# Kernel tuning notes

Hardware: AMD Instinct MI355X
Metric: run time of the kernel (lower is better)

The kernel has to match this reference:

```python
import jax, jax.numpy as jnp
import numpy as np

B, T, J, D_O = 32, 128, 16, 16
D, H, L, M = 256, 8, 4, 8
DH = D // H
GMAX = 5
MLP = 4 * D
NUM_JOINT = np.array([16, 12, 10, 14, 16, 8, 12, 16])
NUM_GLOBAL = np.array([4, 0, 3, 5, 2, 0, 4, 3])


def setup_inputs() -> dict:
    key = jax.random.key(0)
    it = iter(jax.random.split(key, 48))
    def nrm(shape, s):
        return jax.random.normal(next(it), shape, dtype=jnp.float32) * s
    obs = jax.random.normal(next(it), (B, T, J, D_O), dtype=jnp.float32)
    jtype = jax.random.randint(next(it), (B, T, J), 0, 3)
    slide_mask = jtype == 0
    hinge_mask = jtype == 1
    global_mask = jtype == 2
    act_mask = jax.random.randint(next(it), (B, T, J), 0, 2).astype(bool)
    morph_mask = jax.random.randint(next(it), (B, J, J), 0, 2).astype(bool) | jnp.eye(J, dtype=bool)[None]
    m_idx = jax.random.randint(next(it), (B,), 0, M)
    has_global = jnp.asarray(NUM_GLOBAL > 0)
    s = 0.02
    W_slide = nrm((2, D), s); b_slide = jnp.zeros((D,), jnp.float32)
    W_hinge = nrm((3, D), s); b_hinge = jnp.zeros((D,), jnp.float32)
    # per-morphology global projection, rows beyond num_global zeroed (padding)
    grow = jnp.arange(GMAX)[None, :] < jnp.asarray(NUM_GLOBAL)[:, None]
    W_global = nrm((M, GMAX, D), s) * grow[:, :, None]
    b_global = jnp.zeros((M, D), jnp.float32)
    W_act = nrm((1, D), s)  # actuator_embedding: Linear(1, D, bias=False)
    # per-morphology position embeddings, zero beyond num_joint (matches torch zeros init + slice assign)
    jrow = jnp.arange(J)[None, :] < jnp.asarray(NUM_JOINT)[:, None]
    pos_emb = nrm((M, J, D), 1.0) * jrow[:, :, None]
    ln1_w = jnp.ones((L, D), jnp.float32); ln1_b = jnp.zeros((L, D), jnp.float32)
    qkv_w = nrm((L, D, 3 * D), s); qkv_b = jnp.zeros((L, 3 * D), jnp.float32)
    proj_w = nrm((L, D, D), s); proj_b = jnp.zeros((L, D), jnp.float32)
    ln2_w = jnp.ones((L, D), jnp.float32); ln2_b = jnp.zeros((L, D), jnp.float32)
    fc1_w = nrm((L, D, MLP), s); fc1_b = jnp.zeros((L, MLP), jnp.float32)
    fc2_w = nrm((L, MLP, D), s); fc2_b = jnp.zeros((L, D), jnp.float32)
    ls1 = jnp.full((L, D), 1e-4, jnp.float32); ls2 = jnp.full((L, D), 1e-4, jnp.float32)
    return dict(obs=obs, slide_mask=slide_mask, hinge_mask=hinge_mask, global_mask=global_mask,
                act_mask=act_mask, morph_mask=morph_mask, m_idx=m_idx, has_global=has_global,
                W_slide=W_slide, b_slide=b_slide, W_hinge=W_hinge, b_hinge=b_hinge,
                W_global=W_global, b_global=b_global, W_act=W_act, pos_emb=pos_emb,
                ln1_w=ln1_w, ln1_b=ln1_b, qkv_w=qkv_w, qkv_b=qkv_b, proj_w=proj_w, proj_b=proj_b,
                ln2_w=ln2_w, ln2_b=ln2_b, fc1_w=fc1_w, fc1_b=fc1_b, fc2_w=fc2_w, fc2_b=fc2_b,
                ls1=ls1, ls2=ls2)


def _ln(x, w, b):
    m = x.mean(-1, keepdims=True)
    v = ((x - m) ** 2).mean(-1, keepdims=True)
    return (x - m) * jax.lax.rsqrt(v + 1e-5) * w + b


def reference(obs, slide_mask, hinge_mask, global_mask, act_mask, morph_mask, m_idx, has_global,
              W_slide, b_slide, W_hinge, b_hinge, W_global, b_global, W_act, pos_emb,
              ln1_w, ln1_b, qkv_w, qkv_b, proj_w, proj_b, ln2_w, ln2_b,
              fc1_w, fc1_b, fc2_w, fc2_b, ls1, ls2):
    # --- JointEmbedding (morphology-indexed expert selection, vectorized gather) ---
    emb_slide = obs[..., :2] @ W_slide + b_slide
    x = jnp.where(slide_mask[..., None], emb_slide, jnp.zeros_like(emb_slide))
    emb_hinge = obs[..., :3] @ W_hinge + b_hinge
    x = jnp.where(hinge_mask[..., None], emb_hinge, x)
    # per-sample expert weights gathered by m_idx; padded cols are zero so math matches per-expert in-dims
    emb_g = jnp.einsum('btjg,bgd->btjd', obs[..., :GMAX], W_global[m_idx]) + b_global[m_idx][:, None, None, :]
    gmask = global_mask & has_global[m_idx][:, None, None]  # experts with num_global==0 are skipped
    x = jnp.where(gmask[..., None], emb_g, x)
    # actuator embedding: Linear(1, D, bias=False) on 0/1 mask
    x = x + act_mask[..., None].astype(x.dtype) * W_act[0]
    # morphology-indexed position embedding (zero-padded beyond num_joint)
    x = x + pos_emb[m_idx][:, None]  # (B,1,J,D) broadcast over T
    # --- masked transformer over joints; (B T) flattening == broadcasting mask over T ---
    bias = jnp.where(morph_mask, 0.0, -1e9).astype(x.dtype)[:, None, None, :, :]  # (B,1,1,J,J)
    for l in range(L):
        h = _ln(x, ln1_w[l], ln1_b[l])
        qkv = h @ qkv_w[l] + qkv_b[l]
        q, k, v = jnp.split(qkv, 3, axis=-1)
        def heads(t):
            return t.reshape(B, T, J, H, DH).transpose(0, 1, 3, 2, 4)
        q, k, v = heads(q), heads(k), heads(v)
        scores = jnp.einsum('bthqd,bthkd->bthqk', q, k) * (DH ** -0.5) + bias
        a = jax.nn.softmax(scores, axis=-1)
        o = jnp.einsum('bthqk,bthkd->bthqd', a, v).transpose(0, 1, 3, 2, 4).reshape(B, T, J, D)
        x = x + ls1[l] * (o @ proj_w[l] + proj_b[l])
        h = _ln(x, ln2_w[l], ln2_b[l])
        x = x + ls2[l] * (jax.nn.gelu(h @ fc1_w[l] + fc1_b[l]) @ fc2_w[l] + fc2_b[l])
    return x
```

## Files before the change

### kernel.cpp

```cpp
#include <hip/hip_runtime.h>
#include <hip/hip_bf16.h>
#include <stdint.h>

typedef short bf16x8 __attribute__((ext_vector_type(8)));
typedef float f32x4 __attribute__((ext_vector_type(4)));

#define DI __device__ __forceinline__

DI unsigned short f2bf(float f) {
    return __builtin_bit_cast(unsigned short, __float2bfloat16(f));
}

DI unsigned char f2fp8(float f) {
    int p = __builtin_amdgcn_cvt_pk_fp8_f32(f, 0.f, 0, false);
    return (unsigned char)(p & 0xff);
}

DI f32x4 mfma16(bf16x8 a, bf16x8 b, f32x4 c) {
    return __builtin_amdgcn_mfma_f32_16x16x32_bf16(a, b, c, 0, 0, 0);
}

DI f32x4 mfma8(long a, long b, f32x4 c) {
    return __builtin_amdgcn_mfma_f32_16x16x32_fp8_fp8(a, b, c, 0, 0, 0);
}

DI void gload16c(const unsigned char* g, unsigned char* l) {
    __builtin_amdgcn_global_load_lds(
        (const __attribute__((address_space(1))) unsigned int*)g,
        (__attribute__((address_space(3))) unsigned int*)l, 16, 0, 0);
}

DI float gelu_s(float hv) {
    return hv / (1.0f + __expf(-1.702f * hv));
}

#define RSYNC0() do { asm volatile("s_waitcnt vmcnt(0)" ::: "memory"); \
    __builtin_amdgcn_s_barrier(); __builtin_amdgcn_sched_barrier(0); } while (0)

__global__ __launch_bounds__(256)
void prep_kernel(const float* __restrict__ qkv_w, const float* __restrict__ proj_w,
                 const float* __restrict__ fc1_w, const float* __restrict__ fc2_w,
                 const float* __restrict__ ls1, const float* __restrict__ ls2,
                 unsigned char* __restrict__ out)
{
    __shared__ float tileA[256][17];
    __shared__ float tileB[32][129];
    const int tid = threadIdx.x;
    const int tgl = blockIdx.x;
    const int layer = tgl / 192;
    const int tl = tgl % 192;
    bool kindA; const float* W; int ldN = 0, src_n16 = 0, strip = 0, ctb = 0;
    const float* lsp = nullptr;
    size_t off;
    if (tl < 64) {
        int h = tl >> 3, u = tl & 7;
        if (u < 6) { kindA = true;  W = qkv_w + (size_t)layer * 256 * 768; ldN = 768;
                     src_n16 = (u >> 1) * 16 + 2 * h + (u & 1);
                     off = (size_t)h * 40960 + (u < 4 ? u * 4096 : 16384 + (u - 4) * 4096); }
        else       { kindA = false; W = proj_w + (size_t)layer * 256 * 256; ldN = 256;
                     strip = 32 * h; ctb = (u - 6) * 8; lsp = ls1 + layer * 256;
                     off = (size_t)h * 40960 + 24576 + (size_t)(u - 6) * 8192; }
    } else {
        int q = tl - 64, rp = q >> 2, v = q & 3;
        if (v < 2) { kindA = true;  W = fc1_w + (size_t)layer * 256 * 1024; ldN = 1024;
                     src_n16 = 2 * rp + v;
                     off = 327680 + (size_t)rp * 24576 + (size_t)v * 4096; }
        else       { kindA = false; W = fc2_w + (size_t)layer * 1024 * 256; ldN = 256;
                     strip = 32 * rp; ctb = (v - 2) * 8; lsp = ls2 + layer * 256;
                     off = 327680 + (size_t)rp * 24576 + 8192 + (size_t)(v - 2) * 8192; }
    }
    off += (size_t)layer * 1114112;
    if (kindA) {
        const int cn = tid & 15, k0 = tid >> 4;
        const float* src = W + src_n16 * 16 + cn;
        #pragma unroll
        for (int p = 0; p < 16; ++p) {
            int kk = p * 16 + k0;
            tileA[kk][cn] = src[(size_t)kk * ldN];
        }
    } else {
        const int kk = tid >> 3, c0 = (tid & 7) * 16;
        const float* src = W + (size_t)(strip + kk) * ldN + ctb * 16 + c0;
        #pragma unroll
        for (int j = 0; j < 16; ++j) tileB[kk][c0 + j] = src[j];
    }
    __syncthreads();
    if (kindA) {
        unsigned char* dstb = out + off;
        int e0 = tid * 16;
        int s = e0 >> 9;
        int l = (e0 >> 3) & 63;
        union { unsigned char u[8]; unsigned long long v; } g0, g1;
        int kb0 = 32 * s + 8 * (l >> 4), n0 = l & 15;
        int kb1 = 32 * s + 8 * ((l + 1) >> 4), n1 = (l + 1) & 15;
        #pragma unroll
        for (int i = 0; i < 8; ++i) g0.u[i] = f2fp8(tileA[kb0 + i][n0]);
        #pragma unroll
        for (int i = 0; i < 8; ++i) g1.u[i] = f2fp8(tileA[kb1 + i][n1]);
        *(unsigned long long*)(dstb + e0) = g0.v;
        *(unsigned long long*)(dstb + e0 + 8) = g1.v;
    } else {
        unsigned short* dsts = (unsigned short*)(out + off);
        int e0 = tid * 16;
        int s = e0 >> 9;
        int l = (e0 >> 3) & 63;
        union { unsigned short u[8]; bf16x8 v; } pk;
        {
            int kb = 8 * (l >> 4);
            int cc = s * 16 + (l & 15);
            const float sc = lsp[ctb * 16 + cc];
            #pragma unroll
            for (int i = 0; i < 8; ++i) pk.u[i] = f2bf(tileB[kb + i][cc] * sc);
            *(bf16x8*)(dsts + e0) = pk.v;
        }
        int e1 = e0 + 8;
        int s1 = e1 >> 9;
        int l1 = (e1 >> 3) & 63;
        union { unsigned short u[8]; bf16x8 v; } pk1;
        {
            int kb = 8 * (l1 >> 4);
            int cc = s1 * 16 + (l1 & 15);
            const float sc = lsp[ctb * 16 + cc];
            #pragma unroll
            for (int i = 0; i < 8; ++i) pk1.u[i] = f2bf(tileB[kb + i][cc] * sc);
            *(bf16x8*)(dsts + e1) = pk1.v;
        }
    }
}

#define CAT_(a, b) a##b
#define CAT(a, b) CAT_(a, b)

#define F8N(F)      F(0)F(1)F(2)F(3)F(4)F(5)F(6)F(7)
#define F16N(F)     F(0)F(1)F(2)F(3)F(4)F(5)F(6)F(7)F(8)F(9)F(10)F(11)F(12)F(13)F(14)F(15)
#define F8A(F,a)    F(0,a)F(1,a)F(2,a)F(3,a)F(4,a)F(5,a)F(6,a)F(7,a)
#define F8H(F,a)    F(8,a)F(9,a)F(10,a)F(11,a)F(12,a)F(13,a)F(14,a)F(15,a)
#define F16A(F,a)   F8A(F,a) F8H(F,a)
#define F8B(F,a,b)  F(0,a,b)F(1,a,b)F(2,a,b)F(3,a,b)F(4,a,b)F(5,a,b)F(6,a,b)F(7,a,b)
#define F16C(F,a,b) F8B(F,a,b) F(8,a,b)F(9,a,b)F(10,a,b)F(11,a,b)F(12,a,b)F(13,a,b)F(14,a,b)F(15,a,b)

#define DECLX(n)  f32x4 CAT(xA,n);
#define DECLAV(s) long CAT(avA,s);

#define EMB_N(n, P, R) { const int col = (n)*16 + lq; float e = 0.f;            \
    if (sl_) e = o0_*W_slide[col] + o1_*W_slide[256+col] + b_slide[col];        \
    else if (hi_) e = o0_*W_hinge[col] + o1_*W_hinge[256+col]                   \
                    + o2_*W_hinge[512+col] + b_hinge[col];                      \
    else if (gl_) e = b_global[m*256+col]                                       \
        + o0_*W_global[(m*5+0)*256+col] + o1_*W_global[(m*5+1)*256+col]         \
        + o2_*W_global[(m*5+2)*256+col] + o3_*W_global[(m*5+3)*256+col]         \
        + o4_*W_global[(m*5+4)*256+col];                                        \
    if (am_) e += W_act[col];                                                   \
    e += pos_emb[pb_ + col];                                                    \
    CAT(CAT(x,P),n)[R] = e; }

#define EMB_ROW(R, G, P) { const int j_ = lg*4 + (R);                           \
    const size_t tok_ = (size_t)(G)*16 + j_;                                    \
    const float* ob_ = obs + tok_*16;                                           \
    const float o0_=ob_[0], o1_=ob_[1], o2_=ob_[2], o3_=ob_[3], o4_=ob_[4];     \
    const int sl_=slide_m[tok_], hi_=hinge_m[tok_];                             \
    const int gl_=global_m[tok_]&&hg; const int am_=act_m[tok_];                \
    const size_t pb_ = ((size_t)m*16+j_)*256;                                   \
    F16C(EMB_N, P, R) }

#define EMBED(G, P) { EMB_ROW(0,G,P) EMB_ROW(1,G,P) EMB_ROW(2,G,P) EMB_ROW(3,G,P) }

#define LNS_N(n, P) { f32x4 v4_ = CAT(CAT(x,P),n);                              \
    sm0+=v4_[0]; sq0+=v4_[0]*v4_[0]; sm1+=v4_[1]; sq1+=v4_[1]*v4_[1];           \
    sm2+=v4_[2]; sq2+=v4_[2]*v4_[2]; sm3+=v4_[3]; sq3+=v4_[3]*v4_[3]; }

#define RED4(v) { v+=__shfl_xor(v,1,64); v+=__shfl_xor(v,2,64);                 \
                  v+=__shfl_xor(v,4,64); v+=__shfl_xor(v,8,64); }

#define LNW_N(n, P) { const float wv_=lw_[(n)*16+lq], lbv_=lb_[(n)*16+lq];      \
    const int t16_=(2*(n)+(lq>>3))&3; const int base_=(((n)&7)>>1)*512+(lq&7);  \
    slotA8[base_+(4*lg+0+16*t16_)*8] = f2fp8((CAT(CAT(x,P),n)[0]-mu0)*rs0*wv_+lbv_); \
    slotA8[base_+(4*lg+1+16*t16_)*8] = f2fp8((CAT(CAT(x,P),n)[1]-mu1)*rs1*wv_+lbv_); \
    slotA8[base_+(4*lg+2+16*t16_)*8] = f2fp8((CAT(CAT(x,P),n)[2]-mu2)*rs2*wv_+lbv_); \
    slotA8[base_+(4*lg+3+16*t16_)*8] = f2fp8((CAT(CAT(x,P),n)[3]-mu3)*rs3*wv_+lbv_); }

#define LAYER_NORM(LW, LB, P) do {                                              \
    const float* lw_ = (LW); const float* lb_ = (LB);                           \
    float sm0=0,sm1=0,sm2=0,sm3=0, sq0=0,sq1=0,sq2=0,sq3=0;                     \
    F16A(LNS_N, P)                                                              \
    RED4(sm0) RED4(sm1) RED4(sm2) RED4(sm3)                                     \
    RED4(sq0) RED4(sq1) RED4(sq2) RED4(sq3)                                     \
    const float mu0=sm0*(1.f/256.f), mu1=sm1*(1.f/256.f);                       \
    const float mu2=sm2*(1.f/256.f), mu3=sm3*(1.f/256.f);                       \
    const float rs0=rsqrtf(sq0*(1.f/256.f)-mu0*mu0+1e-5f);                      \
    const float rs1=rsqrtf(sq1*(1.f/256.f)-mu1*mu1+1e-5f);                      \
    const float rs2=rsqrtf(sq2*(1.f/256.f)-mu2*mu2+1e-5f);                      \
    const float rs3=rsqrtf(sq3*(1.f/256.f)-mu3*mu3+1e-5f);                      \
    F8A(LNW_N, P)                                                               \
    CAT(CAT(av,P),0) = *(const long*)(slotA8 + 0*512 + lane*8);                 \
    CAT(CAT(av,P),1) = *(const long*)(slotA8 + 1*512 + lane*8);                 \
    CAT(CAT(av,P),2) = *(const long*)(slotA8 + 2*512 + lane*8);                 \
    CAT(CAT(av,P),3) = *(const long*)(slotA8 + 3*512 + lane*8);                 \
    F8H(LNW_N, P)                                                               \
    CAT(CAT(av,P),4) = *(const long*)(slotA8 + 0*512 + lane*8);                 \
    CAT(CAT(av,P),5) = *(const long*)(slotA8 + 1*512 + lane*8);                 \
    CAT(CAT(av,P),6) = *(const long*)(slotA8 + 2*512 + lane*8);                 \
    CAT(CAT(av,P),7) = *(const long*)(slotA8 + 3*512 + lane*8);                 \
} while (0)

#define MFKE(s, TB_) { ae = mfma8(CAT(avA,s), bfragW8((TB_),(s)), ae); }
#define MFKO(s, TB_) { aod = mfma8(CAT(avA,s), bfragW8((TB_),(s)), aod); }
#define MFK8F(TB_) MFKE(0,TB_) MFKO(1,TB_) MFKE(2,TB_) MFKO(3,TB_) \
                   MFKE(4,TB_) MFKO(5,TB_) MFKE(6,TB_) MFKO(7,TB_)

#define FOLD_CT(ct, SB, OF) {                                                   \
    bf16x8 bq_ = *(const bf16x8*)(dbuf + (SB) + ((ct)>>3)*8192                  \
                                  + ((ct)&7)*1024 + lane*16);                   \
    CAT(xA,ct) = mfma16((OF), bq_, CAT(xA,ct)); }

#define ADDB_N(n, OFS) { const float d_ = biasbuf[(OFS)+(n)*16+lq];             \
    CAT(xA,n)[0]+=d_; CAT(xA,n)[1]+=d_; CAT(xA,n)[2]+=d_; CAT(xA,n)[3]+=d_; }

#define STORE_N(n) {                                                            \
    op0[(lg*4+0)*256+(n)*16+lq]=CAT(xA,n)[0]; op0[(lg*4+1)*256+(n)*16+lq]=CAT(xA,n)[1]; \
    op0[(lg*4+2)*256+(n)*16+lq]=CAT(xA,n)[2]; op0[(lg*4+3)*256+(n)*16+lq]=CAT(xA,n)[3]; }

#define ATTN_ROUND(RR, BB) {                                                    \
    const int rg_ = layer * 24 + (RR);                                          \
    RSYNC0();                                                                   \
    if (rg_ + 1 < 96) stageRound(rg_ + 1);                                      \
    _Pragma("unroll")                                                           \
    for (int tt = 0; tt < 4; ++tt) {                                            \
        int sec = tt >> 1, nn = tt & 1;                                         \
        float bv = biasbuf[sec * 256 + (2 * (RR) + nn) * 16 + lq];              \
        f32x4 ae = {bv, bv, bv, bv}, aod = zf;                                  \
        MFK8F((BB) + tt * 4096)                                                 \
        f32x4 a0 = ae + aod;                                                    \
        unsigned short* dstl = sec ? ks : qp;                                   \
        _Pragma("unroll")                                                       \
        for (int rr = 0; rr < 4; ++rr)                                          \
            dstl[(4 * lg + rr) * 40 + nn * 16 + lq] = f2bf(a0[rr]);             \
    }                                                                           \
    _Pragma("unroll")                                                           \
    for (int tv = 0; tv < 2; ++tv) {                                            \
        float bv = biasbuf[512 + (2 * (RR) + tv) * 16 + lq];                    \
        f32x4 ae = {bv, bv, bv, bv}, aod = zf;                                  \
        MFK8F((BB) + 16384 + tv * 4096)                                         \
        f32x4 a0 = ae + aod;                                                    \
        _Pragma("unroll")                                                       \
        for (int rr = 0; rr < 4; ++rr)                                          \
            vT[(tv * 16 + lq) * 40 + 4 * lg + rr] = f2bf(a0[rr]);               \
    }                                                                           \
    { bf16x8 of_ = attn(); F16C(FOLD_CT, (BB) + 24576, of_) }                   \
}

#define MLP_ROUND(RR, BB) {                                                     \
    const int rg_ = layer * 24 + 8 + (RR);                                      \
    RSYNC0();                                                                   \
    if (rg_ + 1 < 96) stageRound(rg_ + 1);                                      \
    _Pragma("unroll")                                                           \
    for (int u = 0; u < 2; ++u) {                                               \
        const int ub_ = (BB) + u * 24576;                                       \
        const int rp_ = 2 * (RR) + u;                                           \
        _Pragma("unroll")                                                       \
        for (int tt = 0; tt < 2; ++tt) {                                        \
            float bv = biasbuf[768 + (2 * rp_ + tt) * 16 + lq];                 \
            f32x4 ae = {bv, bv, bv, bv}, aod = zf;                              \
            MFK8F(ub_ + tt * 4096)                                              \
            f32x4 a0 = ae + aod;                                                \
            int t16 = (2 * tt + (lq >> 3)) & 3;                                 \
            _Pragma("unroll")                                                   \
            for (int rr = 0; rr < 4; ++rr)                                      \
                ks[((4 * lg + rr) + 16 * t16) * 8 + (lq & 7)]                   \
                    = f2bf(gelu_s(a0[rr]));                                     \
        }                                                                       \
        bf16x8 gf_ = *(const bf16x8*)(ks + lane * 8);                           \
        F16C(FOLD_CT, ub_ + 8192, gf_)                                          \
    }                                                                           \
}

__global__ __launch_bounds__(512)
void fused_kernel(const float* __restrict__ obs, const int* __restrict__ slide_m,
                  const int* __restrict__ hinge_m, const int* __restrict__ global_m,
                  const int* __restrict__ act_m, const int* __restrict__ morph_m,
                  const int* __restrict__ m_idx, const int* __restrict__ has_g,
                  const float* __restrict__ W_slide, const float* __restrict__ b_slide,
                  const float* __restrict__ W_hinge, const float* __restrict__ b_hinge,
                  const float* __restrict__ W_global, const float* __restrict__ b_global,
                  const float* __restrict__ W_act, const float* __restrict__ pos_emb,
                  const float* __restrict__ ln1_w, const float* __restrict__ ln1_b,
                  const float* __restrict__ qkv_b, const float* __restrict__ proj_b,
                  const float* __restrict__ ln2_w, const float* __restrict__ ln2_b,
                  const float* __restrict__ fc1_b, const float* __restrict__ fc2_b,
                  const float* __restrict__ ls1, const float* __restrict__ ls2,
                  const unsigned char* __restrict__ wsb, float* __restrict__ out)
{
    __shared__ __align__(16) unsigned char smem[151552];
    unsigned char* dbuf = smem;
    float* bias_lds = (float*)(smem + 98304);
    float* biasbuf = (float*)(smem + 99328);
    const int tid = threadIdx.x;
    const int w = tid >> 6, lane = tid & 63, lq = lane & 15, lg = lane >> 4;
    unsigned char* pw = smem + 108544 + w * 5376;
    unsigned char* slotA8 = pw;
    unsigned short* qp = (unsigned short*)pw;
    unsigned short* ks = (unsigned short*)(pw + 1280);
    unsigned short* vT = (unsigned short*)(pw + 2560);

    const int G = blockIdx.x * 8 + w;
    const int b = blockIdx.x >> 4;
    const int m = m_idx[b];
    const int hg = has_g[m];

    auto bfragW8 = [&](int tb, int s) -> long {
        return *(const long*)(dbuf + tb + s * 512 + lane * 8);
    };
    auto stageRound = [&](int ri) {
        int lyr = ri / 24, rr = ri - lyr * 24;
        size_t off; int nld;
        if (rr < 8) { off = (size_t)lyr * 1114112 + (size_t)rr * 40960; nld = 5; }
        else        { off = (size_t)lyr * 1114112 + 327680 + (size_t)(rr - 8) * 49152;
                      nld = 6; }
        const unsigned char* src = wsb + off + tid * 16;
        unsigned char* dst = dbuf + (ri & 1) * 49152 + tid * 16;
        gload16c(src, dst);
        gload16c(src + 8192, dst + 8192);
        gload16c(src + 16384, dst + 16384);
        gload16c(src + 24576, dst + 24576);
        gload16c(src + 32768, dst + 32768);
        if (nld == 6) gload16c(src + 40960, dst + 40960);
    };

    stageRound(0);
    if (tid < 256) bias_lds[tid] = morph_m[b * 256 + tid] ? 0.0f : -1e9f;
    #pragma unroll
    for (int ii = 0; ii < 8; ++ii) {
        int idx = ii * 64 + lane;
        vT[(idx >> 4) * 40 + 16 + (idx & 15)] = 0;
    }

    F16N(DECLX)
    F8N(DECLAV)

    EMBED(G, A)

    const float SCALE = 0.17677669529663687f;
    const f32x4 zf = {0.f, 0.f, 0.f, 0.f};

    auto attn = [&]() -> bf16x8 {
        bf16x8 kf = *(const bf16x8*)(ks + lq * 40 + lg * 8);
        bf16x8 qf = *(const bf16x8*)(qp + lq * 40 + lg * 8);
        f32x4 st = mfma16(kf, qf, zf);
        float p0 = st[0] * SCALE + bias_lds[lq * 16 + 4 * lg + 0];
        float p1 = st[1] * SCALE + bias_lds[lq * 16 + 4 * lg + 1];
        float p2 = st[2] * SCALE + bias_lds[lq * 16 + 4 * lg + 2];
        float p3 = st[3] * SCALE + bias_lds[lq * 16 + 4 * lg + 3];
        float mx = fmaxf(fmaxf(p0, p1), fmaxf(p2, p3));
        mx = fmaxf(mx, __shfl_xor(mx, 16, 64));
        mx = fmaxf(mx, __shfl_xor(mx, 32, 64));
        p0 = __expf(p0 - mx); p1 = __expf(p1 - mx);
        p2 = __expf(p2 - mx); p3 = __expf(p3 - mx);
        float ps = p0 + p1 + p2 + p3;
        ps += __shfl_xor(ps, 16, 64);
        ps += __shfl_xor(ps, 32, 64);
        float inv = 1.f / ps;
        qp[lq * 40 + lg * 4 + 0] = f2bf(p0 * inv);
        qp[lq * 40 + lg * 4 + 1] = f2bf(p1 * inv);
        qp[lq * 40 + lg * 4 + 2] = f2bf(p2 * inv);
        qp[lq * 40 + lg * 4 + 3] = f2bf(p3 * inv);
        qp[lq * 40 + 16 + lg * 4 + 0] = 0;
        qp[lq * 40 + 16 + lg * 4 + 1] = 0;
        qp[lq * 40 + 16 + lg * 4 + 2] = 0;
        qp[lq * 40 + 16 + lg * 4 + 3] = 0;
        bf16x8 pf = *(const bf16x8*)(qp + lq * 40 + lg * 8);
        f32x4 o0 = mfma16(pf, *(const bf16x8*)(vT + lq * 40 + lg * 8), zf);
        f32x4 o1 = mfma16(pf, *(const bf16x8*)(vT + (16 + lq) * 40 + lg * 8), zf);
        #pragma unroll
        for (int rr = 0; rr < 4; ++rr) {
            ks[((4 * lg + rr) + 16 * ((lq >> 3) & 3)) * 8 + (lq & 7)] = f2bf(o0[rr]);
            ks[((4 * lg + rr) + 16 * ((2 + (lq >> 3)) & 3)) * 8 + (lq & 7)] = f2bf(o1[rr]);
        }
        return *(const bf16x8*)(ks + lane * 8);
    };

    for (int layer = 0; layer < 4; ++layer) {
        for (int i = tid; i < 2304; i += 512) {
            float v;
            if (i < 768)       v = qkv_b[layer * 768 + i];
            else if (i < 1792) v = fc1_b[layer * 1024 + i - 768];
            else if (i < 2048) v = ls1[layer * 256 + i - 1792] * proj_b[layer * 256 + i - 1792];
            else               v = ls2[layer * 256 + i - 2048] * fc2_b[layer * 256 + i - 2048];
            biasbuf[i] = v;
        }
        __syncthreads();

        LAYER_NORM(ln1_w + layer * 256, ln1_b + layer * 256, A);
        #pragma unroll
        for (int ii = 0; ii < 8; ++ii) {
            int idx = ii * 64 + lane;
            vT[(idx >> 4) * 40 + 16 + (idx & 15)] = 0;
        }
        F16A(ADDB_N, 1792)

        for (int hp = 0; hp < 4; ++hp) {
            ATTN_ROUND(2 * hp, 0)
            ATTN_ROUND(2 * hp + 1, 49152)
        }

        LAYER_NORM(ln2_w + layer * 256, ln2_b + layer * 256, A);
        F16A(ADDB_N, 2048)

        for (int mp = 0; mp < 8; ++mp) {
            MLP_ROUND(2 * mp, 0)
            MLP_ROUND(2 * mp + 1, 49152)
        }
    }

    float* op0 = out + (size_t)G * 4096;
    F16N(STORE_N)
}

extern "C" void kernel_launch(void* const* d_in, const int* in_sizes, int n_in,
                              void* d_out, int out_size, void* d_ws, size_t ws_size,
                              hipStream_t stream) {
    (void)in_sizes; (void)n_in; (void)out_size; (void)ws_size;
    const float* obs      = (const float*)d_in[0];
    const int*   slide_m  = (const int*)d_in[1];
    const int*   hinge_m  = (const int*)d_in[2];
    const int*   global_m = (const int*)d_in[3];
    const int*   act_m    = (const int*)d_in[4];
    const int*   morph_m  = (const int*)d_in[5];
    const int*   m_idx    = (const int*)d_in[6];
    const int*   has_g    = (const int*)d_in[7];
    const float* W_slide  = (const float*)d_in[8];
    const float* b_slide  = (const float*)d_in[9];
    const float* W_hinge  = (const float*)d_in[10];
    const float* b_hinge  = (const float*)d_in[11];
    const float* W_global = (const float*)d_in[12];
    const float* b_global = (const float*)d_in[13];
    const float* W_act    = (const float*)d_in[14];
    const float* pos_emb  = (const float*)d_in[15];
    const float* ln1_w    = (const float*)d_in[16];
    const float* ln1_b    = (const float*)d_in[17];
    const float* qkv_w    = (const float*)d_in[18];
    const float* qkv_b    = (const float*)d_in[19];
    const float* proj_w   = (const float*)d_in[20];
    const float* proj_b   = (const float*)d_in[21];
    const float* ln2_w    = (const float*)d_in[22];
    const float* ln2_b    = (const float*)d_in[23];
    const float* fc1_w    = (const float*)d_in[24];
    const float* fc1_b    = (const float*)d_in[25];
    const float* fc2_w    = (const float*)d_in[26];
    const float* fc2_b    = (const float*)d_in[27];
    const float* ls1      = (const float*)d_in[28];
    const float* ls2      = (const float*)d_in[29];
    unsigned char* wsb = (unsigned char*)d_ws;

    prep_kernel<<<768, 256, 0, stream>>>(qkv_w, proj_w, fc1_w, fc2_w, ls1, ls2, wsb);
    fused_kernel<<<512, 512, 0, stream>>>(obs, slide_m, hinge_m, global_m, act_m, morph_m,
        m_idx, has_g, W_slide, b_slide, W_hinge, b_hinge, W_global, b_global, W_act, pos_emb,
        ln1_w, ln1_b, qkv_b, proj_b, ln2_w, ln2_b, fc1_b, fc2_b, ls1, ls2, wsb, (float*)d_out);
}
```

Before: 618.4 us.

## Interleave FP8 weight fragments for 16-byte LDS loads and use four accumulators

The weight-prep kernel now writes the FP8 B-fragments so that k-slices 2p and 2p+1 for a lane sit next to each other. The main kernel can then fetch two fragments with one 16-byte LDS read instead of two 8-byte reads. The MFMA chain is also split across four accumulators instead of two, which shortens dependency chains. The cost is extra accumulator registers and a packed layout that the preprocessing and the consumer must agree on exactly.

Measured after the change: 621.6 us. About the same (+0.5%).

```diff
diff --git a/kernel.cpp b/kernel.cpp
--- a/kernel.cpp
+++ b/kernel.cpp
@@ -4,6 +4,7 @@
 
 typedef short bf16x8 __attribute__((ext_vector_type(8)));
 typedef float f32x4 __attribute__((ext_vector_type(4)));
+typedef long longx2 __attribute__((ext_vector_type(2)));
 
 #define DI __device__ __forceinline__
 
@@ -87,18 +88,17 @@
     __syncthreads();
     if (kindA) {
         unsigned char* dstb = out + off;
-        int e0 = tid * 16;
-        int s = e0 >> 9;
-        int l = (e0 >> 3) & 63;
+        const int p = tid >> 6, l = tid & 63;
+        const int s0 = 2 * p, s1 = 2 * p + 1;
         union { unsigned char u[8]; unsigned long long v; } g0, g1;
-        int kb0 = 32 * s + 8 * (l >> 4), n0 = l & 15;
-        int kb1 = 32 * s + 8 * ((l + 1) >> 4), n1 = (l + 1) & 15;
+        int kb0 = 32 * s0 + 8 * (l >> 4), n0 = l & 15;
+        int kb1 = 32 * s1 + 8 * (l >> 4), n1 = l & 15;
         #pragma unroll
         for (int i = 0; i < 8; ++i) g0.u[i] = f2fp8(tileA[kb0 + i][n0]);
         #pragma unroll
         for (int i = 0; i < 8; ++i) g1.u[i] = f2fp8(tileA[kb1 + i][n1]);
-        *(unsigned long long*)(dstb + e0) = g0.v;
-        *(unsigned long long*)(dstb + e0 + 8) = g1.v;
+        *(unsigned long long*)(dstb + tid * 16) = g0.v;
+        *(unsigned long long*)(dstb + tid * 16 + 8) = g1.v;
     } else {
         unsigned short* dsts = (unsigned short*)(out + off);
         int e0 = tid * 16;
@@ -203,10 +203,15 @@
     CAT(CAT(av,P),7) = *(const long*)(slotA8 + 3*512 + lane*8);                 \
 } while (0)
 
-#define MFKE(s, TB_) { ae = mfma8(CAT(avA,s), bfragW8((TB_),(s)), ae); }
-#define MFKO(s, TB_) { aod = mfma8(CAT(avA,s), bfragW8((TB_),(s)), aod); }
-#define MFK8F(TB_) MFKE(0,TB_) MFKO(1,TB_) MFKE(2,TB_) MFKO(3,TB_) \
-                   MFKE(4,TB_) MFKO(5,TB_) MFKE(6,TB_) MFKO(7,TB_)
+#define MFK8F(TB_) {                                                            \
+    longx2 b01_ = *(const longx2*)(dbuf + (TB_) + 0 * 1024 + lane * 16);        \
+    longx2 b23_ = *(const longx2*)(dbuf + (TB_) + 1 * 1024 + lane * 16);        \
+    longx2 b45_ = *(const longx2*)(dbuf + (TB_) + 2 * 1024 + lane * 16);        \
+    longx2 b67_ = *(const longx2*)(dbuf + (TB_) + 3 * 1024 + lane * 16);        \
+    ac0 = mfma8(avA0, b01_[0], ac0); ac1 = mfma8(avA1, b01_[1], ac1);           \
+    ac2 = mfma8(avA2, b23_[0], ac2); ac3 = mfma8(avA3, b23_[1], ac3);           \
+    ac0 = mfma8(avA4, b45_[0], ac0); ac1 = mfma8(avA5, b45_[1], ac1);           \
+    ac2 = mfma8(avA6, b67_[0], ac2); ac3 = mfma8(avA7, b67_[1], ac3); }
 
 #define FOLD_CT(ct, SB, OF) {                                                   \
     bf16x8 bq_ = *(const bf16x8*)(dbuf + (SB) + ((ct)>>3)*8192                  \
@@ -228,9 +233,9 @@
     for (int tt = 0; tt < 4; ++tt) {                                            \
         int sec = tt >> 1, nn = tt & 1;                                         \
         float bv = biasbuf[sec * 256 + (2 * (RR) + nn) * 16 + lq];              \
-        f32x4 ae = {bv, bv, bv, bv}, aod = zf;                                  \
+        f32x4 ac0 = {bv, bv, bv, bv}, ac1 = zf, ac2 = zf, ac3 = zf;             \
         MFK8F((BB) + tt * 4096)                                                 \
-        f32x4 a0 = ae + aod;                                                    \
+        f32x4 a0 = (ac0 + ac1) + (ac2 + ac3);                                   \
         unsigned short* dstl = sec ? ks : qp;                                   \
         _Pragma("unroll")                                                       \
         for (int rr = 0; rr < 4; ++rr)                                          \
@@ -239,9 +244,9 @@
     _Pragma("unroll")                                                           \
     for (int tv = 0; tv < 2; ++tv) {                                            \
         float bv = biasbuf[512 + (2 * (RR) + tv) * 16 + lq];                    \
-        f32x4 ae = {bv, bv, bv, bv}, aod = zf;                                  \
+        f32x4 ac0 = {bv, bv, bv, bv}, ac1 = zf, ac2 = zf, ac3 = zf;             \
         MFK8F((BB) + 16384 + tv * 4096)                                         \
-        f32x4 a0 = ae + aod;                                                    \
+        f32x4 a0 = (ac0 + ac1) + (ac2 + ac3);                                   \
         _Pragma("unroll")                                                       \
         for (int rr = 0; rr < 4; ++rr)                                          \
             vT[(tv * 16 + lq) * 40 + 4 * lg + rr] = f2bf(a0[rr]);               \
@@ -260,9 +265,9 @@
         _Pragma("unroll")                                                       \
         for (int tt = 0; tt < 2; ++tt) {                                        \
             float bv = biasbuf[768 + (2 * rp_ + tt) * 16 + lq];                 \
-            f32x4 ae = {bv, bv, bv, bv}, aod = zf;                              \
+            f32x4 ac0 = {bv, bv, bv, bv}, ac1 = zf, ac2 = zf, ac3 = zf;         \
             MFK8F(ub_ + tt * 4096)                                              \
-            f32x4 a0 = ae + aod;                                                \
+            f32x4 a0 = (ac0 + ac1) + (ac2 + ac3);                               \
             int t16 = (2 * tt + (lq >> 3)) & 3;                                 \
             _Pragma("unroll")                                                   \
             for (int rr = 0; rr < 4; ++rr)                                      \
@@ -307,9 +312,6 @@
     const int m = m_idx[b];
     const int hg = has_g[m];
 
-    auto bfragW8 = [&](int tb, int s) -> long {
-        return *(const long*)(dbuf + tb + s * 512 + lane * 8);
-    };
     auto stageRound = [&](int ri) {
         int lyr = ri / 24, rr = ri - lyr * 24;
         size_t off; int nld;
```
